# Optimization experiments

Hardware: AMD Instinct MI355X
Metric: run time of the kernel (lower is better)

Reference implementation:

```python
import jax, jax.numpy as jnp
import numpy as np

EMBED_DIM = 1024
NUM_HEADS = 16
HEAD_DIM = EMBED_DIM // NUM_HEADS
B, S = 2, 2048


def setup_inputs() -> dict:
    key = jax.random.key(0)
    ks = jax.random.split(key, 10)
    inp = {
        "query": jax.random.normal(ks[0], (B, S, EMBED_DIM), dtype=jnp.float32),
        "key": jax.random.normal(ks[1], (B, S, EMBED_DIM), dtype=jnp.float32),
        "value": jax.random.normal(ks[2], (B, S, EMBED_DIM), dtype=jnp.float32),
        # 0 => masked key position (matches attn_mask == 0 in the torch code)
        "attn_mask": jax.random.randint(ks[3], (B, S), 0, 2, dtype=jnp.int32),
        "Wq": jax.random.normal(ks[4], (EMBED_DIM, EMBED_DIM), dtype=jnp.float32) * 0.02,
        "bq": jnp.zeros((EMBED_DIM,), dtype=jnp.float32),
        "Wk": jax.random.normal(ks[5], (EMBED_DIM, EMBED_DIM), dtype=jnp.float32) * 0.02,
        "bk": jnp.zeros((EMBED_DIM,), dtype=jnp.float32),
        "Wv": jax.random.normal(ks[6], (EMBED_DIM, EMBED_DIM), dtype=jnp.float32) * 0.02,
        "bv": jnp.zeros((EMBED_DIM,), dtype=jnp.float32),
    }
    return inp


def _proj_heads(x, W, b):
    # x: [B, S, E] -> [B, H, S, D]  (nn.Linear uses x @ W.T + b)
    y = x @ W.T + b
    Bx, Sx, E = y.shape
    return y.reshape(Bx, Sx, NUM_HEADS, HEAD_DIM).transpose(0, 2, 1, 3)


def reference(query, key, value, attn_mask, Wq, bq, Wk, bk, Wv, bv):
    q = _proj_heads(query, Wq, bq)   # [B,H,S,D]
    k = _proj_heads(key, Wk, bk)     # [B,H,S,D]
    v = _proj_heads(value, Wv, bv)   # [B,H,S,D]
    inv_scale = float(EMBED_DIM) ** 0.5  # NOTE: original divides by sqrt(embed_dim), not sqrt(head_dim)
    scores = jnp.einsum("bhqd,bhkd->bhqk", q, k) / inv_scale  # [B,H,S,S]
    mask = (attn_mask == 0)[:, None, None, :]  # [B,1,1,S] -> broadcast over [B,H,S,S]
    scores = jnp.where(mask, -jnp.inf, scores)
    attn = jax.nn.softmax(scores, axis=-1)
    # dropout omitted for deterministic reference (see notes)
    out = jnp.einsum("bhqk,bhkd->bhqd", attn, v)  # [B,H,S,D]
    return out
```

## Files before the change

kernel.cpp:

```cpp
#include <hip/hip_runtime.h>
#include <hip/hip_bf16.h>

constexpr int BB = 2;
constexpr int SS = 2048;
constexpr int EE = 1024;
constexpr int HH = 16;
constexpr int DD = 64;
constexpr int MM = BB * SS;
constexpr int CX = MM * EE;
constexpr int CW = EE * EE;
#define QSCALE 0.045084220027780106f

typedef __attribute__((ext_vector_type(8))) short short8;
typedef __attribute__((ext_vector_type(4))) float floatx4;
typedef __attribute__((ext_vector_type(4))) unsigned uintx4;

union fragu { uintx4 u; short8 s; };

__device__ inline short bf16bits(float x) {
    __hip_bfloat16 h = __float2bfloat16(x);
    return *reinterpret_cast<short*>(&h);
}

__device__ inline unsigned pkbf(float a, float b) {
    return (unsigned)(unsigned short)bf16bits(a) |
           ((unsigned)(unsigned short)bf16bits(b) << 16);
}

__device__ inline float fast_exp2(float x) {
#if __has_builtin(__builtin_amdgcn_exp2f)
    return __builtin_amdgcn_exp2f(x);
#else
    return exp2f(x);
#endif
}

__device__ inline void gl_lds16(const __hip_bfloat16* g, const short* l) {
    __builtin_amdgcn_global_load_lds(
        (const __attribute__((address_space(1))) void*)g,
        (__attribute__((address_space(3))) void*)l, 16, 0, 0);
}

__device__ inline int sigma_row(int p) {
    return (p & 0x23) | ((p & 0x0C) << 1) | ((p & 0x10) >> 2);
}

#define TURN4 { __asm__ volatile("s_waitcnt vmcnt(4)" ::: "memory"); __builtin_amdgcn_s_barrier(); }
#define TURN0 { __asm__ volatile("s_waitcnt vmcnt(0)" ::: "memory"); __builtin_amdgcn_s_barrier(); }

__global__ __launch_bounds__(256) void convert_kernel(
    const float* __restrict__ x0, const float* __restrict__ x1, const float* __restrict__ x2,
    const float* __restrict__ w0, const float* __restrict__ w1, const float* __restrict__ w2,
    __hip_bfloat16* __restrict__ xb, __hip_bfloat16* __restrict__ wb)
{
    const long long e = (long long)(blockIdx.x * 256 + threadIdx.x) * 8;
    const float* src;
    __hip_bfloat16* dst;
    if (e < 3LL * CX) {
        const int z = (int)(e >> 22);
        const int off = (int)(e & (CX - 1));
        src = ((z == 0) ? x0 : (z == 1) ? x1 : x2) + off;
        dst = xb + e;
    } else {
        const long long e2 = e - 3LL * CX;
        const int z = (int)(e2 >> 20);
        const int off = (int)(e2 & (CW - 1));
        src = ((z == 0) ? w0 : (z == 1) ? w1 : w2) + off;
        dst = wb + e2;
    }
    const float4 a = reinterpret_cast<const float4*>(src)[0];
    const float4 b = reinterpret_cast<const float4*>(src)[1];
    short8 r;
    r[0] = bf16bits(a.x); r[1] = bf16bits(a.y); r[2] = bf16bits(a.z); r[3] = bf16bits(a.w);
    r[4] = bf16bits(b.x); r[5] = bf16bits(b.y); r[6] = bf16bits(b.z); r[7] = bf16bits(b.w);
    *reinterpret_cast<short8*>(dst) = r;
}

__global__ __launch_bounds__(256) void proj_gemm(
    const __hip_bfloat16* __restrict__ xb,
    const __hip_bfloat16* __restrict__ wb,
    const float* __restrict__ bq, const float* __restrict__ bk, const float* __restrict__ bv,
    __hip_bfloat16* __restrict__ qws,
    __hip_bfloat16* __restrict__ kws,
    __hip_bfloat16* __restrict__ vtws)
{
    const int which = blockIdx.z;
    const __hip_bfloat16* A = xb + (size_t)which * CX;
    const __hip_bfloat16* W = wb + (size_t)which * CW;
    const float* bias = (which == 0) ? bq : (which == 1) ? bk : bv;

    const int m0   = blockIdx.x * 128;
    const int n0   = blockIdx.y * 128;
    const int tid  = threadIdx.x;
    const int wave = tid >> 6;
    const int lane = tid & 63;
    const int l15  = lane & 15;
    const int quad = lane >> 4;
    const int wr   = wave >> 1;
    const int wc   = wave & 1;

    __shared__ __align__(16) short As[128 * 32];
    __shared__ __align__(16) short Bs[128 * 32];

    const int dpos  = (lane & 7) ^ (lane >> 3);
    const int drloc = 2 * (lane >> 3) + (dpos >> 2);
    const int dgran = (dpos & 3) * 8;

    const int rbase = (l15 >> 1) * 64;
    const int rslot = (((l15 & 1) * 4 + quad) ^ (l15 >> 1)) * 8;

    floatx4 acc[4][4] = {};

    for (int k0 = 0; k0 < EE; k0 += 32) {
        __syncthreads();
        #pragma unroll
        for (int p = 0; p < 2; ++p) {
            const int rb16 = wave * 32 + p * 16;
            gl_lds16(A + (size_t)(m0 + rb16 + drloc) * EE + k0 + dgran, &As[rb16 * 32]);
            gl_lds16(W + (size_t)(n0 + rb16 + drloc) * EE + k0 + dgran, &Bs[rb16 * 32]);
        }
        __syncthreads();

        short8 af[4], bf[4];
        #pragma unroll
        for (int mt = 0; mt < 4; ++mt)
            af[mt] = *reinterpret_cast<const short8*>(
                &As[(wr * 32 + mt * 8) * 64 + rbase + rslot]);
        #pragma unroll
        for (int nt = 0; nt < 4; ++nt)
            bf[nt] = *reinterpret_cast<const short8*>(
                &Bs[(wc * 32 + nt * 8) * 64 + rbase + rslot]);

        #pragma unroll
        for (int mt = 0; mt < 4; ++mt)
            #pragma unroll
            for (int nt = 0; nt < 4; ++nt)
                acc[mt][nt] = __builtin_amdgcn_mfma_f32_16x16x32_bf16(af[mt], bf[nt], acc[mt][nt], 0, 0, 0);
    }

    #pragma unroll
    for (int nt = 0; nt < 4; ++nt) {
        const int n = n0 + wc * 64 + nt * 16 + l15;
        const float bval = bias[n];
        const int h = n >> 6, d = n & 63;
        #pragma unroll
        for (int mt = 0; mt < 4; ++mt) {
            #pragma unroll
            for (int r = 0; r < 4; ++r) {
                const int m = m0 + wr * 64 + mt * 16 + quad * 4 + r;
                const int b = m >> 11;
                const int s = m & (SS - 1);
                float val = acc[mt][nt][r] + bval;
                if (which == 0) val *= QSCALE;
                const __hip_bfloat16 hv = __float2bfloat16(val);
                if (which == 0)
                    qws[(((size_t)b * HH + h) * SS + s) * DD + d] = hv;
                else if (which == 1)
                    kws[(((size_t)b * HH + h) * SS + s) * DD + d] = hv;
                else
                    vtws[(((size_t)b * HH + h) * DD + d) * SS + s] = hv;
            }
        }
    }
}

#define ATTN_PF(B, T) { \
    const int kn = (T) * 64; \
    gl_lds16(Kg + (size_t)(kn + sk0) * DD + sg, Ksg + (B) * 4096 + rb0 * 64); \
    gl_lds16(VTg + (size_t)(rb0 + srow) * SS + kn + sg, Vsg + (B) * 4096 + rb0 * 64); \
    gl_lds16(Kg + (size_t)(kn + sk1) * DD + sg, Ksg + (B) * 4096 + rb1 * 64); \
    gl_lds16(VTg + (size_t)(rb1 + srow) * SS + kn + sg, Vsg + (B) * 4096 + rb1 * 64); }

#define ATTN_BODY(B, T) { \
    const int kt = (T) * 64; \
    floatx4 s[4][4]; \
    __builtin_amdgcn_s_setprio(1); \
    _Pragma("unroll") \
    for (int f = 0; f < 4; ++f) { \
        const int krow = (f * 16 + l15) * 64; \
        const short8 ka = *reinterpret_cast<const short8*>(Ksg + (B) * 4096 + krow + (quad ^ swz) * 8); \
        const short8 kb = *reinterpret_cast<const short8*>(Ksg + (B) * 4096 + krow + ((quad + 4) ^ swz) * 8); \
        const float4 mf = *reinterpret_cast<const float4*>( \
            Msb + kt + 32 * (f >> 1) + 8 * quad + 4 * (f & 1)); \
        floatx4 mb; mb[0] = mf.x; mb[1] = mf.y; mb[2] = mf.z; mb[3] = mf.w; \
        _Pragma("unroll") \
        for (int qb = 0; qb < 4; ++qb) { \
            floatx4 z = __builtin_amdgcn_mfma_f32_16x16x32_bf16(ka, qa[qb][0], mb, 0, 0, 0); \
            s[qb][f]  = __builtin_amdgcn_mfma_f32_16x16x32_bf16(kb, qa[qb][1], z, 0, 0, 0); \
        } \
    } \
    __builtin_amdgcn_s_setprio(0); \
    fragu pk[4][2]; \
    _Pragma("unroll") \
    for (int qb = 0; qb < 4; ++qb) \
        _Pragma("unroll") \
        for (int f = 0; f < 4; ++f) { \
            const float e0 = fast_exp2(s[qb][f][0]); \
            const float e1 = fast_exp2(s[qb][f][1]); \
            const float e2 = fast_exp2(s[qb][f][2]); \
            const float e3 = fast_exp2(s[qb][f][3]); \
            const int i0 = (f & 1) * 2; \
            pk[qb][f >> 1].u[i0]     = pkbf(e0, e1); \
            pk[qb][f >> 1].u[i0 + 1] = pkbf(e2, e3); \
        } \
    __builtin_amdgcn_s_setprio(1); \
    _Pragma("unroll") \
    for (int qb = 0; qb < 4; ++qb) { \
        accl[qb] = __builtin_amdgcn_mfma_f32_16x16x32_bf16(pk[qb][0].s, ones, accl[qb], 0, 0, 0); \
        accl[qb] = __builtin_amdgcn_mfma_f32_16x16x32_bf16(pk[qb][1].s, ones, accl[qb], 0, 0, 0); \
    } \
    _Pragma("unroll") \
    for (int nt = 0; nt < 4; ++nt) { \
        const int vrow = (nt * 16 + l15) * 64; \
        const short8 vb0 = *reinterpret_cast<const short8*>(Vsg + (B) * 4096 + vrow + (quad ^ swz) * 8); \
        const short8 vb1 = *reinterpret_cast<const short8*>(Vsg + (B) * 4096 + vrow + ((quad + 4) ^ swz) * 8); \
        _Pragma("unroll") \
        for (int qb = 0; qb < 4; ++qb) { \
            acc[qb][nt] = __builtin_amdgcn_mfma_f32_16x16x32_bf16(pk[qb][0].s, vb0, acc[qb][nt], 0, 0, 0); \
            acc[qb][nt] = __builtin_amdgcn_mfma_f32_16x16x32_bf16(pk[qb][1].s, vb1, acc[qb][nt], 0, 0, 0); \
        } \
    } \
    __builtin_amdgcn_s_setprio(0); }

__global__ __launch_bounds__(512, 2) void attn_kernel(
    const __hip_bfloat16* __restrict__ qws,
    const __hip_bfloat16* __restrict__ kws,
    const __hip_bfloat16* __restrict__ vtws,
    const int* __restrict__ amask,
    float* __restrict__ out)
{
    const int flatb = blockIdx.y * gridDim.x + blockIdx.x;
    const int bh    = 4 * (flatb & 7) + ((flatb >> 3) & 3);
    const int b     = bh >> 4;
    const int q0    = (flatb >> 5) * 256;
    const int tid  = threadIdx.x;
    const int wave = tid >> 6;
    const int lane = tid & 63;
    const int l15  = lane & 15;
    const int quad = lane >> 4;
    const int qg   = wave & 3;
    const int kh   = wave >> 2;

    const __hip_bfloat16* Q   = qws  + (size_t)bh * SS * DD;
    const __hip_bfloat16* Kg  = kws  + (size_t)bh * SS * DD + (size_t)kh * 1024 * DD;
    const __hip_bfloat16* VTg = vtws + (size_t)bh * DD * SS + (size_t)kh * 1024;
    const int* msk = amask + b * SS;

    __shared__ __align__(16) short SM[16 * 4096 + 4096];
    short* Ksg = &SM[kh * 4 * 4096];
    short* Vsg = &SM[(8 + kh * 4) * 4096];
    float* Msf = reinterpret_cast<float*>(&SM[16 * 4096]);
    const float* Msb = Msf + kh * 1024;

    {
        const int4 m4 = reinterpret_cast<const int4*>(msk)[tid];
        float4 f4;
        f4.x = m4.x ? 0.f : -1e30f;
        f4.y = m4.y ? 0.f : -1e30f;
        f4.z = m4.z ? 0.f : -1e30f;
        f4.w = m4.w ? 0.f : -1e30f;
        reinterpret_cast<float4*>(Msf)[tid] = f4;
    }

    const int qrow = q0 + qg * 64 + l15;
    short8 qa[4][2];
    #pragma unroll
    for (int qb = 0; qb < 4; ++qb) {
        qa[qb][0] = *reinterpret_cast<const short8*>(Q + (size_t)(qrow + qb * 16) * DD + quad * 8);
        qa[qb][1] = *reinterpret_cast<const short8*>(Q + (size_t)(qrow + qb * 16) * DD + 32 + quad * 8);
    }

    const int swz = l15 & 7;

    short8 ones;
    #pragma unroll
    for (int i = 0; i < 8; ++i) ones[i] = (short)0x3F80;

    const int srow = lane >> 3;
    const int sg   = ((lane & 7) ^ srow) * 8;
    const int rb0  = qg * 16, rb1 = rb0 + 8;
    const int sk0  = sigma_row(rb0 + srow);
    const int sk1  = sigma_row(rb1 + srow);

    floatx4 acc[4][4] = {};
    floatx4 accl[4] = {};

    ATTN_PF(0, 0);
    ATTN_PF(1, 1);
    __asm__ volatile("s_waitcnt vmcnt(4) lgkmcnt(0)" ::: "memory");
    __builtin_amdgcn_s_barrier();

    for (int t = 0; t < 12; t += 4) {
        ATTN_PF(2, t + 2); ATTN_BODY(0, t);     TURN4;
        ATTN_PF(3, t + 3); ATTN_BODY(1, t + 1); TURN4;
        ATTN_PF(0, t + 4); ATTN_BODY(2, t + 2); TURN4;
        ATTN_PF(1, t + 5); ATTN_BODY(3, t + 3); TURN4;
    }
    ATTN_PF(2, 14); ATTN_BODY(0, 12); TURN4;
    ATTN_PF(3, 15); ATTN_BODY(1, 13); TURN4;
    ATTN_BODY(2, 14); TURN0;
    ATTN_BODY(3, 15);

    __syncthreads();
    float* CB = reinterpret_cast<float*>(&SM[0]);
    float* R  = CB + qg * 5120;
    if (kh == 1) {
        #pragma unroll
        for (int qb = 0; qb < 4; ++qb)
            #pragma unroll
            for (int nt = 0; nt < 4; ++nt)
                *reinterpret_cast<floatx4*>(R + ((qb * 4 + nt) * 64 + lane) * 4) = acc[qb][nt];
        #pragma unroll
        for (int qb = 0; qb < 4; ++qb)
            *reinterpret_cast<floatx4*>(R + ((16 + qb) * 64 + lane) * 4) = accl[qb];
    }
    __syncthreads();
    if (kh == 0) {
        #pragma unroll
        for (int qb = 0; qb < 4; ++qb)
            #pragma unroll
            for (int nt = 0; nt < 4; ++nt) {
                const floatx4 p = *reinterpret_cast<const floatx4*>(R + ((qb * 4 + nt) * 64 + lane) * 4);
                acc[qb][nt][0] += p[0]; acc[qb][nt][1] += p[1];
                acc[qb][nt][2] += p[2]; acc[qb][nt][3] += p[3];
            }
        const size_t obase = (size_t)bh * SS * DD;
        #pragma unroll
        for (int qb = 0; qb < 4; ++qb) {
            const floatx4 pl = *reinterpret_cast<const floatx4*>(R + ((16 + qb) * 64 + lane) * 4);
            float inv[4];
            #pragma unroll
            for (int r = 0; r < 4; ++r)
                inv[r] = 1.f / (accl[qb][r] + pl[r]);
            #pragma unroll
            for (int nt = 0; nt < 4; ++nt)
                #pragma unroll
                for (int r = 0; r < 4; ++r) {
                    const int qq = q0 + qg * 64 + qb * 16 + quad * 4 + r;
                    const int d  = nt * 16 + l15;
                    out[obase + (size_t)qq * DD + d] = acc[qb][nt][r] * inv[r];
                }
        }
    }
}

extern "C" void kernel_launch(void* const* d_in, const int* in_sizes, int n_in,
                              void* d_out, int out_size, void* d_ws, size_t ws_size,
                              hipStream_t stream) {
    const float* q    = (const float*)d_in[0];
    const float* k    = (const float*)d_in[1];
    const float* v    = (const float*)d_in[2];
    const int*   mask = (const int*)d_in[3];
    const float* Wq   = (const float*)d_in[4];
    const float* bq   = (const float*)d_in[5];
    const float* Wk   = (const float*)d_in[6];
    const float* bk   = (const float*)d_in[7];
    const float* Wv   = (const float*)d_in[8];
    const float* bv   = (const float*)d_in[9];
    float* out = (float*)d_out;

    __hip_bfloat16* qws  = (__hip_bfloat16*)d_ws;
    __hip_bfloat16* kws  = qws + (size_t)CX;
    __hip_bfloat16* vtws = kws + (size_t)CX;
    __hip_bfloat16* xb   = vtws + (size_t)CX;
    __hip_bfloat16* wb   = xb + (size_t)3 * CX;

    const int cvt_blocks = (3 * CX + 3 * CW) / (256 * 8);
    convert_kernel<<<dim3(cvt_blocks), 256, 0, stream>>>(q, k, v, Wq, Wk, Wv, xb, wb);
    proj_gemm<<<dim3(MM / 128, EE / 128, 3), 256, 0, stream>>>(
        xb, wb, bq, bk, bv, qws, kws, vtws);
    attn_kernel<<<dim3(SS / 256, BB * HH), 512, 0, stream>>>(
        qws, kws, vtws, mask, out);
}
```

Before: 196.1 us.

## Software-pipeline attention loop so QK of the next tile overlaps PV

Splits the per-tile attention body into three stages: QK score MFMAs, the exp/pack softmax step, and PV MFMAs. The loop is rescheduled so the QK for tile t+1 and the PV for tile t run in the same step, with two ping-pong packed-probability buffers, so the exp/pack VALU work can overlap with matrix-core work. It also loads the mask bias directly as a vector type instead of copying it element by element. The cost is more live registers (a second pk buffer plus the score array) under a 512-thread, 2-blocks-per-CU launch bound, which risks spills or lower occupancy.

```diff
diff --git a/kernel.cpp b/kernel.cpp
--- a/kernel.cpp
+++ b/kernel.cpp
@@ -171,26 +171,25 @@
     gl_lds16(Kg + (size_t)(kn + sk1) * DD + sg, Ksg + (B) * 4096 + rb1 * 64); \
     gl_lds16(VTg + (size_t)(rb1 + srow) * SS + kn + sg, Vsg + (B) * 4096 + rb1 * 64); }
 
-#define ATTN_BODY(B, T) { \
+#define ATTN_QK(B, T) { \
     const int kt = (T) * 64; \
-    floatx4 s[4][4]; \
     __builtin_amdgcn_s_setprio(1); \
     _Pragma("unroll") \
     for (int f = 0; f < 4; ++f) { \
         const int krow = (f * 16 + l15) * 64; \
         const short8 ka = *reinterpret_cast<const short8*>(Ksg + (B) * 4096 + krow + (quad ^ swz) * 8); \
         const short8 kb = *reinterpret_cast<const short8*>(Ksg + (B) * 4096 + krow + ((quad + 4) ^ swz) * 8); \
-        const float4 mf = *reinterpret_cast<const float4*>( \
+        const floatx4 mb = *reinterpret_cast<const floatx4*>( \
             Msb + kt + 32 * (f >> 1) + 8 * quad + 4 * (f & 1)); \
-        floatx4 mb; mb[0] = mf.x; mb[1] = mf.y; mb[2] = mf.z; mb[3] = mf.w; \
         _Pragma("unroll") \
         for (int qb = 0; qb < 4; ++qb) { \
             floatx4 z = __builtin_amdgcn_mfma_f32_16x16x32_bf16(ka, qa[qb][0], mb, 0, 0, 0); \
             s[qb][f]  = __builtin_amdgcn_mfma_f32_16x16x32_bf16(kb, qa[qb][1], z, 0, 0, 0); \
         } \
     } \
-    __builtin_amdgcn_s_setprio(0); \
-    fragu pk[4][2]; \
+    __builtin_amdgcn_s_setprio(0); }
+
+#define ATTN_SM(PK) { \
     _Pragma("unroll") \
     for (int qb = 0; qb < 4; ++qb) \
         _Pragma("unroll") \
@@ -200,14 +199,16 @@
             const float e2 = fast_exp2(s[qb][f][2]); \
             const float e3 = fast_exp2(s[qb][f][3]); \
             const int i0 = (f & 1) * 2; \
-            pk[qb][f >> 1].u[i0]     = pkbf(e0, e1); \
-            pk[qb][f >> 1].u[i0 + 1] = pkbf(e2, e3); \
-        } \
+            PK[qb][f >> 1].u[i0]     = pkbf(e0, e1); \
+            PK[qb][f >> 1].u[i0 + 1] = pkbf(e2, e3); \
+        } }
+
+#define ATTN_PV(B, PK) { \
     __builtin_amdgcn_s_setprio(1); \
     _Pragma("unroll") \
     for (int qb = 0; qb < 4; ++qb) { \
-        accl[qb] = __builtin_amdgcn_mfma_f32_16x16x32_bf16(pk[qb][0].s, ones, accl[qb], 0, 0, 0); \
-        accl[qb] = __builtin_amdgcn_mfma_f32_16x16x32_bf16(pk[qb][1].s, ones, accl[qb], 0, 0, 0); \
+        accl[qb] = __builtin_amdgcn_mfma_f32_16x16x32_bf16(PK[qb][0].s, ones, accl[qb], 0, 0, 0); \
+        accl[qb] = __builtin_amdgcn_mfma_f32_16x16x32_bf16(PK[qb][1].s, ones, accl[qb], 0, 0, 0); \
     } \
     _Pragma("unroll") \
     for (int nt = 0; nt < 4; ++nt) { \
@@ -216,8 +217,8 @@
         const short8 vb1 = *reinterpret_cast<const short8*>(Vsg + (B) * 4096 + vrow + ((quad + 4) ^ swz) * 8); \
         _Pragma("unroll") \
         for (int qb = 0; qb < 4; ++qb) { \
-            acc[qb][nt] = __builtin_amdgcn_mfma_f32_16x16x32_bf16(pk[qb][0].s, vb0, acc[qb][nt], 0, 0, 0); \
-            acc[qb][nt] = __builtin_amdgcn_mfma_f32_16x16x32_bf16(pk[qb][1].s, vb1, acc[qb][nt], 0, 0, 0); \
+            acc[qb][nt] = __builtin_amdgcn_mfma_f32_16x16x32_bf16(PK[qb][0].s, vb0, acc[qb][nt], 0, 0, 0); \
+            acc[qb][nt] = __builtin_amdgcn_mfma_f32_16x16x32_bf16(PK[qb][1].s, vb1, acc[qb][nt], 0, 0, 0); \
         } \
     } \
     __builtin_amdgcn_s_setprio(0); }
@@ -284,22 +285,25 @@
 
     floatx4 acc[4][4] = {};
     floatx4 accl[4] = {};
+    floatx4 s[4][4];
+    fragu pkA[4][2], pkB[4][2];
 
     ATTN_PF(0, 0);
     ATTN_PF(1, 1);
     __asm__ volatile("s_waitcnt vmcnt(4) lgkmcnt(0)" ::: "memory");
     __builtin_amdgcn_s_barrier();
 
-    for (int t = 0; t < 12; t += 4) {
-        ATTN_PF(2, t + 2); ATTN_BODY(0, t);     TURN4;
-        ATTN_PF(3, t + 3); ATTN_BODY(1, t + 1); TURN4;
-        ATTN_PF(0, t + 4); ATTN_BODY(2, t + 2); TURN4;
-        ATTN_PF(1, t + 5); ATTN_BODY(3, t + 3); TURN4;
-    }
-    ATTN_PF(2, 14); ATTN_BODY(0, 12); TURN4;
-    ATTN_PF(3, 15); ATTN_BODY(1, 13); TURN4;
-    ATTN_BODY(2, 14); TURN0;
-    ATTN_BODY(3, 15);
+    ATTN_PF(2, 2); ATTN_QK(0, 0); ATTN_SM(pkA); TURN4;
+    ATTN_PF(3, 3); ATTN_QK(1, 1); ATTN_PV(0, pkA); ATTN_SM(pkB); TURN4;
+    for (int t = 2; t < 14; t += 4) {
+        ATTN_PF(0, t + 2); ATTN_QK(2, t);     ATTN_PV(1, pkB); ATTN_SM(pkA); TURN4;
+        ATTN_PF(1, t + 3); ATTN_QK(3, t + 1); ATTN_PV(2, pkA); ATTN_SM(pkB); TURN4;
+        ATTN_PF(2, t + 4); ATTN_QK(0, t + 2); ATTN_PV(3, pkB); ATTN_SM(pkA); TURN4;
+        ATTN_PF(3, t + 5); ATTN_QK(1, t + 3); ATTN_PV(0, pkA); ATTN_SM(pkB); TURN4;
+    }
+    ATTN_QK(2, 14); ATTN_PV(1, pkB); ATTN_SM(pkA); TURN0;
+    ATTN_QK(3, 15); ATTN_PV(2, pkA); ATTN_SM(pkB);
+    ATTN_PV(3, pkB);
 
     __syncthreads();
     float* CB = reinterpret_cast<float*>(&SM[0]);
```

After: 202.2 us. +3.1%, slower.

## Software-pipeline attention loop so QK of next tile overlaps PV of previous

Applied to the files above, without the earlier changes.

Splits the attention body into QK, softmax-exp and PV stages and reorders the loop so the QK MFMAs for tile t+1 are issued before the PV MFMAs for tile t. Each PV reads the probabilities packed in the previous iteration, so exp work can overlap matrix-core work within a wave. Holding the extra live scores and packed probabilities raises register pressure, so launch bounds drop from 2 to 1 block per CU, which halves occupancy. The pipeline has an extra prologue and epilogue stage, and PV(3) reuses the LDS buffer of tile 15 after the loop ends.

```diff
diff --git a/kernel.cpp b/kernel.cpp
--- a/kernel.cpp
+++ b/kernel.cpp
@@ -171,26 +171,25 @@
     gl_lds16(Kg + (size_t)(kn + sk1) * DD + sg, Ksg + (B) * 4096 + rb1 * 64); \
     gl_lds16(VTg + (size_t)(rb1 + srow) * SS + kn + sg, Vsg + (B) * 4096 + rb1 * 64); }
 
-#define ATTN_BODY(B, T) { \
+#define ATTN_QK(B, T) { \
     const int kt = (T) * 64; \
-    floatx4 s[4][4]; \
     __builtin_amdgcn_s_setprio(1); \
     _Pragma("unroll") \
     for (int f = 0; f < 4; ++f) { \
         const int krow = (f * 16 + l15) * 64; \
         const short8 ka = *reinterpret_cast<const short8*>(Ksg + (B) * 4096 + krow + (quad ^ swz) * 8); \
         const short8 kb = *reinterpret_cast<const short8*>(Ksg + (B) * 4096 + krow + ((quad + 4) ^ swz) * 8); \
-        const float4 mf = *reinterpret_cast<const float4*>( \
+        const floatx4 mb = *reinterpret_cast<const floatx4*>( \
             Msb + kt + 32 * (f >> 1) + 8 * quad + 4 * (f & 1)); \
-        floatx4 mb; mb[0] = mf.x; mb[1] = mf.y; mb[2] = mf.z; mb[3] = mf.w; \
         _Pragma("unroll") \
         for (int qb = 0; qb < 4; ++qb) { \
             floatx4 z = __builtin_amdgcn_mfma_f32_16x16x32_bf16(ka, qa[qb][0], mb, 0, 0, 0); \
             s[qb][f]  = __builtin_amdgcn_mfma_f32_16x16x32_bf16(kb, qa[qb][1], z, 0, 0, 0); \
         } \
     } \
-    __builtin_amdgcn_s_setprio(0); \
-    fragu pk[4][2]; \
+    __builtin_amdgcn_s_setprio(0); }
+
+#define ATTN_SM { \
     _Pragma("unroll") \
     for (int qb = 0; qb < 4; ++qb) \
         _Pragma("unroll") \
@@ -202,7 +201,9 @@
             const int i0 = (f & 1) * 2; \
             pk[qb][f >> 1].u[i0]     = pkbf(e0, e1); \
             pk[qb][f >> 1].u[i0 + 1] = pkbf(e2, e3); \
-        } \
+        } }
+
+#define ATTN_PV(B) { \
     __builtin_amdgcn_s_setprio(1); \
     _Pragma("unroll") \
     for (int qb = 0; qb < 4; ++qb) { \
@@ -222,7 +223,7 @@
     } \
     __builtin_amdgcn_s_setprio(0); }
 
-__global__ __launch_bounds__(512, 2) void attn_kernel(
+__global__ __launch_bounds__(512, 1) void attn_kernel(
     const __hip_bfloat16* __restrict__ qws,
     const __hip_bfloat16* __restrict__ kws,
     const __hip_bfloat16* __restrict__ vtws,
@@ -284,22 +285,25 @@
 
     floatx4 acc[4][4] = {};
     floatx4 accl[4] = {};
+    floatx4 s[4][4];
+    fragu pk[4][2];
 
     ATTN_PF(0, 0);
     ATTN_PF(1, 1);
     __asm__ volatile("s_waitcnt vmcnt(4) lgkmcnt(0)" ::: "memory");
     __builtin_amdgcn_s_barrier();
 
-    for (int t = 0; t < 12; t += 4) {
-        ATTN_PF(2, t + 2); ATTN_BODY(0, t);     TURN4;
-        ATTN_PF(3, t + 3); ATTN_BODY(1, t + 1); TURN4;
-        ATTN_PF(0, t + 4); ATTN_BODY(2, t + 2); TURN4;
-        ATTN_PF(1, t + 5); ATTN_BODY(3, t + 3); TURN4;
-    }
-    ATTN_PF(2, 14); ATTN_BODY(0, 12); TURN4;
-    ATTN_PF(3, 15); ATTN_BODY(1, 13); TURN4;
-    ATTN_BODY(2, 14); TURN0;
-    ATTN_BODY(3, 15);
+    ATTN_PF(2, 2); ATTN_QK(0, 0); ATTN_SM; TURN4;
+    for (int t = 1; t < 13; t += 4) {
+        ATTN_PF(3, t + 2); ATTN_QK(1, t);     ATTN_PV(0); ATTN_SM; TURN4;
+        ATTN_PF(0, t + 3); ATTN_QK(2, t + 1); ATTN_PV(1); ATTN_SM; TURN4;
+        ATTN_PF(1, t + 4); ATTN_QK(3, t + 2); ATTN_PV(2); ATTN_SM; TURN4;
+        ATTN_PF(2, t + 5); ATTN_QK(0, t + 3); ATTN_PV(3); ATTN_SM; TURN4;
+    }
+    ATTN_PF(3, 15); ATTN_QK(1, 13); ATTN_PV(0); ATTN_SM; TURN4;
+    ATTN_QK(2, 14); ATTN_PV(1); ATTN_SM; TURN0;
+    ATTN_QK(3, 15); ATTN_PV(2); ATTN_SM;
+    ATTN_PV(3);
 
     __syncthreads();
     float* CB = reinterpret_cast<float*>(&SM[0]);
```

After: 252.0 us. 28.5% more time.

## Halve attention block to 128 queries with 4 waves and double-buffered K/V

Applied to the files above, without the earlier changes.

The attention kernel now runs 256-thread blocks covering 128 query rows instead of 512-thread blocks covering 256, doubling the grid. Each wave loads twice as many K/V rows per prefetch. The pipeline shrinks from a 4-deep to a 2-deep LDS ring that waits for all loads at every step. The smaller LDS footprint and block size may let more blocks run per CU and improve load balance, but K/V reuse per block halves and the shallower prefetch exposes more memory latency.

```diff
diff --git a/kernel.cpp b/kernel.cpp
--- a/kernel.cpp
+++ b/kernel.cpp
@@ -45,7 +45,6 @@
     return (p & 0x23) | ((p & 0x0C) << 1) | ((p & 0x10) >> 2);
 }
 
-#define TURN4 { __asm__ volatile("s_waitcnt vmcnt(4)" ::: "memory"); __builtin_amdgcn_s_barrier(); }
 #define TURN0 { __asm__ volatile("s_waitcnt vmcnt(0)" ::: "memory"); __builtin_amdgcn_s_barrier(); }
 
 __global__ __launch_bounds__(256) void convert_kernel(
@@ -166,10 +165,14 @@
 
 #define ATTN_PF(B, T) { \
     const int kn = (T) * 64; \
-    gl_lds16(Kg + (size_t)(kn + sk0) * DD + sg, Ksg + (B) * 4096 + rb0 * 64); \
-    gl_lds16(VTg + (size_t)(rb0 + srow) * SS + kn + sg, Vsg + (B) * 4096 + rb0 * 64); \
-    gl_lds16(Kg + (size_t)(kn + sk1) * DD + sg, Ksg + (B) * 4096 + rb1 * 64); \
-    gl_lds16(VTg + (size_t)(rb1 + srow) * SS + kn + sg, Vsg + (B) * 4096 + rb1 * 64); }
+    gl_lds16(Kg + (size_t)(kn + sk0) * DD + sg, Ksg + (B) * 4096 + rbA * 64); \
+    gl_lds16(VTg + (size_t)(rbA + srow) * SS + kn + sg, Vsg + (B) * 4096 + rbA * 64); \
+    gl_lds16(Kg + (size_t)(kn + sk1) * DD + sg, Ksg + (B) * 4096 + rbB * 64); \
+    gl_lds16(VTg + (size_t)(rbB + srow) * SS + kn + sg, Vsg + (B) * 4096 + rbB * 64); \
+    gl_lds16(Kg + (size_t)(kn + sk2) * DD + sg, Ksg + (B) * 4096 + rbC * 64); \
+    gl_lds16(VTg + (size_t)(rbC + srow) * SS + kn + sg, Vsg + (B) * 4096 + rbC * 64); \
+    gl_lds16(Kg + (size_t)(kn + sk3) * DD + sg, Ksg + (B) * 4096 + rbD * 64); \
+    gl_lds16(VTg + (size_t)(rbD + srow) * SS + kn + sg, Vsg + (B) * 4096 + rbD * 64); }
 
 #define ATTN_BODY(B, T) { \
     const int kt = (T) * 64; \
@@ -222,7 +225,7 @@
     } \
     __builtin_amdgcn_s_setprio(0); }
 
-__global__ __launch_bounds__(512, 2) void attn_kernel(
+__global__ __launch_bounds__(256, 2) void attn_kernel(
     const __hip_bfloat16* __restrict__ qws,
     const __hip_bfloat16* __restrict__ kws,
     const __hip_bfloat16* __restrict__ vtws,
@@ -232,34 +235,36 @@
     const int flatb = blockIdx.y * gridDim.x + blockIdx.x;
     const int bh    = 4 * (flatb & 7) + ((flatb >> 3) & 3);
     const int b     = bh >> 4;
-    const int q0    = (flatb >> 5) * 256;
+    const int q0    = (flatb >> 5) * 128;
     const int tid  = threadIdx.x;
     const int wave = tid >> 6;
     const int lane = tid & 63;
     const int l15  = lane & 15;
     const int quad = lane >> 4;
-    const int qg   = wave & 3;
-    const int kh   = wave >> 2;
+    const int qg   = wave & 1;
+    const int kh   = wave >> 1;
 
     const __hip_bfloat16* Q   = qws  + (size_t)bh * SS * DD;
     const __hip_bfloat16* Kg  = kws  + (size_t)bh * SS * DD + (size_t)kh * 1024 * DD;
     const __hip_bfloat16* VTg = vtws + (size_t)bh * DD * SS + (size_t)kh * 1024;
     const int* msk = amask + b * SS;
 
-    __shared__ __align__(16) short SM[16 * 4096 + 4096];
-    short* Ksg = &SM[kh * 4 * 4096];
-    short* Vsg = &SM[(8 + kh * 4) * 4096];
-    float* Msf = reinterpret_cast<float*>(&SM[16 * 4096]);
+    __shared__ __align__(16) short SM[8 * 4096 + 4096];
+    short* Ksg = &SM[kh * 2 * 4096];
+    short* Vsg = &SM[(4 + kh * 2) * 4096];
+    float* Msf = reinterpret_cast<float*>(&SM[8 * 4096]);
     const float* Msb = Msf + kh * 1024;
 
-    {
-        const int4 m4 = reinterpret_cast<const int4*>(msk)[tid];
+    #pragma unroll
+    for (int i = 0; i < 2; ++i) {
+        const int j = tid + i * 256;
+        const int4 m4 = reinterpret_cast<const int4*>(msk)[j];
         float4 f4;
         f4.x = m4.x ? 0.f : -1e30f;
         f4.y = m4.y ? 0.f : -1e30f;
         f4.z = m4.z ? 0.f : -1e30f;
         f4.w = m4.w ? 0.f : -1e30f;
-        reinterpret_cast<float4*>(Msf)[tid] = f4;
+        reinterpret_cast<float4*>(Msf)[j] = f4;
     }
 
     const int qrow = q0 + qg * 64 + l15;
@@ -278,28 +283,25 @@
 
     const int srow = lane >> 3;
     const int sg   = ((lane & 7) ^ srow) * 8;
-    const int rb0  = qg * 16, rb1 = rb0 + 8;
-    const int sk0  = sigma_row(rb0 + srow);
-    const int sk1  = sigma_row(rb1 + srow);
+    const int rbA  = qg * 32, rbB = rbA + 8, rbC = rbA + 16, rbD = rbA + 24;
+    const int sk0  = sigma_row(rbA + srow);
+    const int sk1  = sigma_row(rbB + srow);
+    const int sk2  = sigma_row(rbC + srow);
+    const int sk3  = sigma_row(rbD + srow);
 
     floatx4 acc[4][4] = {};
     floatx4 accl[4] = {};
 
     ATTN_PF(0, 0);
-    ATTN_PF(1, 1);
-    __asm__ volatile("s_waitcnt vmcnt(4) lgkmcnt(0)" ::: "memory");
+    __asm__ volatile("s_waitcnt vmcnt(0) lgkmcnt(0)" ::: "memory");
     __builtin_amdgcn_s_barrier();
 
-    for (int t = 0; t < 12; t += 4) {
-        ATTN_PF(2, t + 2); ATTN_BODY(0, t);     TURN4;
-        ATTN_PF(3, t + 3); ATTN_BODY(1, t + 1); TURN4;
-        ATTN_PF(0, t + 4); ATTN_BODY(2, t + 2); TURN4;
-        ATTN_PF(1, t + 5); ATTN_BODY(3, t + 3); TURN4;
-    }
-    ATTN_PF(2, 14); ATTN_BODY(0, 12); TURN4;
-    ATTN_PF(3, 15); ATTN_BODY(1, 13); TURN4;
-    ATTN_BODY(2, 14); TURN0;
-    ATTN_BODY(3, 15);
+    for (int t = 0; t < 14; t += 2) {
+        ATTN_PF(1, t + 1); ATTN_BODY(0, t);     TURN0;
+        ATTN_PF(0, t + 2); ATTN_BODY(1, t + 1); TURN0;
+    }
+    ATTN_PF(1, 15); ATTN_BODY(0, 14); TURN0;
+    ATTN_BODY(1, 15);
 
     __syncthreads();
     float* CB = reinterpret_cast<float*>(&SM[0]);
@@ -369,6 +371,6 @@
     convert_kernel<<<dim3(cvt_blocks), 256, 0, stream>>>(q, k, v, Wq, Wk, Wv, xb, wb);
     proj_gemm<<<dim3(MM / 128, EE / 128, 3), 256, 0, stream>>>(
         xb, wb, bq, bk, bv, qws, kws, vtws);
-    attn_kernel<<<dim3(SS / 256, BB * HH), 512, 0, stream>>>(
+    attn_kernel<<<dim3(SS / 128, BB * HH), 256, 0, stream>>>(
         qws, kws, vtws, mask, out);
 }
```

Result: no change. 195.8 us (-0.2%).
